# Kernel tuning notes

Hardware: AMD Instinct MI355X
Metric: run time of the kernel (lower is better)

The kernel has to match this reference:

```python
import jax, jax.numpy as jnp
import numpy as np

B, S, H, HEADS = 4, 4096, 256, 4
DH = H // HEADS
WINDOW = 16
N = B * S
EPS = 1e-5


def _build_edges():
    half = WINDOW // 2
    i = np.arange(S)
    offs = np.concatenate([np.arange(-half, 0), np.arange(1, half)])  # j in [i-half, i+half), j != i
    j = i[:, None] + offs[None, :]
    valid = (j >= 0) & (j < S)
    src_i = np.broadcast_to(i[:, None], j.shape)[valid]
    tgt_j = j[valid]
    w = (1.0 / (1.0 + np.abs(src_i - tgt_j))).astype(np.float32)
    boff = np.arange(B)[:, None] * S
    src = (boff + src_i[None, :]).reshape(-1).astype(np.int32)
    tgt = (boff + tgt_j[None, :]).reshape(-1).astype(np.int32)
    w = np.tile(w, B)
    return src, tgt, w


def setup_inputs() -> dict:
    key = jax.random.key(0)
    ks = jax.random.split(key, 8)
    src, tgt, w = _build_edges()
    sc = 0.02
    return {
        "hidden_states": jax.random.normal(ks[0], (B, S, H), jnp.float32),
        "Wc": jax.random.normal(ks[1], (H, H), jnp.float32) * sc,
        "bc": jnp.zeros((H,), jnp.float32),
        "Wa": jax.random.normal(ks[2], (H, H), jnp.float32) * sc,
        "a_src": jax.random.normal(ks[3], (HEADS, DH), jnp.float32) * sc,
        "a_tgt": jax.random.normal(ks[4], (HEADS, DH), jnp.float32) * sc,
        "ba": jnp.zeros((H,), jnp.float32),
        "ln_g": jnp.ones((H,), jnp.float32),
        "ln_b": jnp.zeros((H,), jnp.float32),
        "Wg": jax.random.normal(ks[5], (2 * H, H), jnp.float32) * sc,
        "bg": jnp.zeros((H,), jnp.float32),
        "Wp": jax.random.normal(ks[6], (H, H), jnp.float32) * sc,
        "bp": jnp.zeros((H,), jnp.float32),
        "edge_weights": jnp.asarray(w),
        "src": jnp.asarray(src),
        "tgt": jnp.asarray(tgt),
    }


def _ln(x, g, b):
    mu = jnp.mean(x, -1, keepdims=True)
    var = jnp.mean((x - mu) ** 2, -1, keepdims=True)
    return (x - mu) * jax.lax.rsqrt(var + EPS) * g + b


def reference(hidden_states, Wc, bc, Wa, a_src, a_tgt, ba, ln_g, ln_b,
              Wg, bg, Wp, bp, edge_weights, src, tgt):
    x = hidden_states.reshape(N, H)

    # --- layer 0: GraphConvolution ---
    support = x @ Wc                                   # [N,H]
    msg = edge_weights[:, None] * support[src]         # [E,H]
    gs = jax.ops.segment_sum(msg, tgt, num_segments=N) + bc
    gs = _ln(gs + x, ln_g, ln_b)

    # --- layer 1: GraphAttention (GAT-style, edge-weighted softmax) ---
    h = (gs @ Wa).reshape(N, HEADS, DH)
    es = jnp.einsum('nhd,hd->nh', h, a_src)            # [N,heads]
    et = jnp.einsum('nhd,hd->nh', h, a_tgt)
    logits = jax.nn.leaky_relu(es[src] + et[tgt], 0.2)  # [E,heads]
    m = jax.ops.segment_max(logits, tgt, num_segments=N)
    un = jnp.exp(logits - m[tgt]) * edge_weights[:, None]
    den = jax.ops.segment_sum(un, tgt, num_segments=N)
    alpha = un / (den[tgt] + 1e-9)                      # [E,heads]
    agg = jax.ops.segment_sum(alpha[:, :, None] * h[src], tgt, num_segments=N)
    gs = agg.reshape(N, H) + ba
    gs = _ln(gs + x, ln_g, ln_b)

    # --- gated integration ---
    gate = jax.nn.sigmoid(jnp.concatenate([x, gs], -1) @ Wg + bg)
    enhanced = x + gate * (gs @ Wp + bp)
    return enhanced.reshape(B, S, H)
```

## Files before the change

kernel.cpp:

```cpp
#include <hip/hip_runtime.h>
#include <math.h>

#define HD 256
#define SEQ 4096
#define NR 16384
#define NHEADS 4
#define EPSV 1e-5f
#define LDP 72
#define ZLDP 264
#define SROWS 32
#define SHALO 15
#define SLDP 264

typedef __attribute__((ext_vector_type(8))) short bf16x8;
typedef __attribute__((ext_vector_type(4))) float f32x4;

__device__ inline short f2bf(float f) {
    unsigned u = __float_as_uint(f);
    u += 0x7FFF + ((u >> 16) & 1);
    return (short)(u >> 16);
}
__device__ inline float bf2f(short s) {
    return __uint_as_float(((unsigned)(unsigned short)s) << 16);
}

__device__ inline void stage_tile(const short* __restrict__ src, int src_stride,
                                  int row0, int k0, short* lds, int rows)
{
    int t = threadIdx.x;
    int nchunk = rows >> 5;
#pragma unroll
    for (int c = 0; c < 8; ++c) {
        if (c >= nchunk) break;
        int idx = c * 256 + t;
        int r = idx >> 3, kg = idx & 7;
        bf16x8 v = *(const bf16x8*)(src + (size_t)(row0 + r) * src_stride + k0 + kg * 8);
        *(bf16x8*)(lds + r * LDP + kg * 8) = v;
    }
}

__global__ __launch_bounds__(256) void prep_w(
    const float* __restrict__ Wc, const float* __restrict__ Wa,
    const float* __restrict__ Wg, const float* __restrict__ Wp,
    short* __restrict__ WcT, short* __restrict__ WaT,
    short* __restrict__ WgT, short* __restrict__ WpT)
{
    __shared__ float lds[64][65];
    int task = blockIdx.y;
    int bx = blockIdx.x;
    int t = threadIdx.x;
    const float* W; short* Wt; int K;
    if (task == 0)      { W = Wc; Wt = WcT; K = 256; }
    else if (task == 1) { W = Wa; Wt = WaT; K = 256; }
    else if (task == 2) { W = Wg; Wt = WgT; K = 512; }
    else                { W = Wp; Wt = WpT; K = 256; }
    int ntiles = (K >> 6) * 4;
    if (bx >= ntiles) return;
    int k0 = (bx >> 2) * 64, n0 = (bx & 3) * 64;
    int ty = t >> 6, tx = t & 63;
#pragma unroll
    for (int s = 0; s < 16; ++s) {
        int r = s * 4 + ty;
        lds[r][tx] = W[(size_t)(k0 + r) * 256 + n0 + tx];
    }
    __syncthreads();
#pragma unroll
    for (int s = 0; s < 16; ++s) {
        int rn = s * 4 + ty;
        Wt[(size_t)(n0 + rn) * K + k0 + tx] = f2bf(lds[tx][rn]);
    }
}

__global__ __launch_bounds__(256) void stencil_gemm(
    const float* __restrict__ x, const short* __restrict__ WcT,
    const float* __restrict__ bc, const short* __restrict__ WaT,
    const float* __restrict__ lng, const float* __restrict__ lnb,
    const float* __restrict__ a_src, const float* __restrict__ a_tgt,
    short* __restrict__ xb, short* __restrict__ hb,
    float* __restrict__ es, float* __restrict__ et)
{
    __shared__ __align__(16) char smem[71168];
    short* lH = (short*)smem;
    short* lB = (short*)smem;
    short* lY = (short*)(smem + 36864);
    short* lZ = (short*)(smem + 53760);
    float* red_s = (float*)(smem + 70656);
    float* red_q = red_s + 64;

    int t = threadIdx.x;
    int bid = blockIdx.x;
    int swz = (bid & 7) * 64 + (bid >> 3);
    int m0 = swz * SROWS;
    int batch_base = m0 & ~(SEQ - 1);

    for (int i = t; i < (SROWS + SHALO) * 64; i += 256) {
        int r = i >> 6, c4 = (i & 63) * 4;
        int grow = m0 - 7 + r;
        short4 o4 = {0, 0, 0, 0};
        if (grow >= batch_base && grow < batch_base + SEQ) {
            float4 v = *(const float4*)(x + (size_t)grow * HD + c4);
            o4.x = f2bf(v.x); o4.y = f2bf(v.y); o4.z = f2bf(v.z); o4.w = f2bf(v.w);
        }
        *(short4*)(lH + r * SLDP + c4) = o4;
    }
    __syncthreads();
    for (int i = t; i < SROWS * 64; i += 256) {
        int r = i >> 6, c4 = (i & 63) * 4;
        *(short4*)(xb + (size_t)(m0 + r) * HD + c4) =
            *(const short4*)(lH + (r + 7) * SLDP + c4);
    }
    {
        int wv = t >> 6, ln_ = t & 63;
        int c0 = ln_ * 4;
        for (int rr = wv; rr < SROWS; rr += 4) {
            float a0 = 0.f, a1 = 0.f, a2 = 0.f, a3 = 0.f;
#pragma unroll
            for (int i = 0; i < 15; ++i) {
                int d = (i < 7) ? (i - 7) : (i - 6);
                float wd = 1.f / (1.f + (float)((d < 0) ? -d : d));
                short4 s4 = *(const short4*)(lH + (rr + 7 + d) * SLDP + c0);
                a0 += wd * bf2f(s4.x); a1 += wd * bf2f(s4.y);
                a2 += wd * bf2f(s4.z); a3 += wd * bf2f(s4.w);
            }
            short4 o;
            o.x = f2bf(a0); o.y = f2bf(a1); o.z = f2bf(a2); o.w = f2bf(a3);
            *(short4*)(lY + rr * ZLDP + c0) = o;
        }
    }

    int lane = t & 63, wid = t >> 6;
    int wm = wid & 1, wn = wid >> 1;
    int lm = lane & 15, lk = (lane >> 4) * 8;
    int rbase = (lane >> 4) * 4;

    f32x4 acc[8] = {};
    for (int kt = 0; kt < 4; ++kt) {
        __syncthreads();
        stage_tile(WcT, HD, 0, kt * 64, lB, 256);
        __syncthreads();
#pragma unroll
        for (int kk2 = 0; kk2 < 64; kk2 += 32) {
            bf16x8 a = *(const bf16x8*)(lY + (wm * 16 + lm) * ZLDP + kt * 64 + kk2 + lk);
#pragma unroll
            for (int j = 0; j < 8; ++j) {
                bf16x8 b = *(const bf16x8*)(lB + (wn * 128 + j * 16 + lm) * LDP + kk2 + lk);
                acc[j] = __builtin_amdgcn_mfma_f32_16x16x32_bf16(a, b, acc[j], 0, 0, 0);
            }
        }
    }
    float zv[8][4];
    float s4r[4] = {}, q4r[4] = {};
#pragma unroll
    for (int j = 0; j < 8; ++j)
#pragma unroll
        for (int r = 0; r < 4; ++r) {
            int n = wn * 128 + j * 16 + lm;
            int row = m0 + wm * 16 + rbase + r;
            float z = acc[j][r] + bc[n] + bf2f(xb[(size_t)row * HD + n]);
            zv[j][r] = z; s4r[r] += z; q4r[r] += z * z;
        }
#pragma unroll
    for (int r = 0; r < 4; ++r)
#pragma unroll
        for (int o = 1; o < 16; o <<= 1) {
            s4r[r] += __shfl_xor(s4r[r], o, 64);
            q4r[r] += __shfl_xor(q4r[r], o, 64);
        }
    if (lm == 0)
#pragma unroll
        for (int r = 0; r < 4; ++r) {
            red_s[wn * 32 + wm * 16 + rbase + r] = s4r[r];
            red_q[wn * 32 + wm * 16 + rbase + r] = q4r[r];
        }
    __syncthreads();
    float mu[4], inv[4];
#pragma unroll
    for (int r = 0; r < 4; ++r) {
        int rowl = wm * 16 + rbase + r;
        float S = red_s[rowl] + red_s[32 + rowl];
        float Q = red_q[rowl] + red_q[32 + rowl];
        mu[r] = S * (1.f / HD);
        inv[r] = rsqrtf(Q * (1.f / HD) - mu[r] * mu[r] + EPSV);
    }
#pragma unroll
    for (int j = 0; j < 8; ++j)
#pragma unroll
        for (int r = 0; r < 4; ++r) {
            int n = wn * 128 + j * 16 + lm;
            int rowl = wm * 16 + rbase + r;
            lZ[rowl * ZLDP + n] = f2bf((zv[j][r] - mu[r]) * inv[r] * lng[n] + lnb[n]);
        }

    f32x4 acc2[8] = {};
    for (int kt = 0; kt < 4; ++kt) {
        __syncthreads();
        stage_tile(WaT, HD, 0, kt * 64, lB, 256);
        __syncthreads();
#pragma unroll
        for (int kk2 = 0; kk2 < 64; kk2 += 32) {
            bf16x8 a = *(const bf16x8*)(lZ + (wm * 16 + lm) * ZLDP + kt * 64 + kk2 + lk);
#pragma unroll
            for (int j = 0; j < 8; ++j) {
                bf16x8 b = *(const bf16x8*)(lB + (wn * 128 + j * 16 + lm) * LDP + kk2 + lk);
                acc2[j] = __builtin_amdgcn_mfma_f32_16x16x32_bf16(a, b, acc2[j], 0, 0, 0);
            }
        }
    }
    float esA[4] = {}, etA[4] = {}, esB[4] = {}, etB[4] = {};
#pragma unroll
    for (int j = 0; j < 8; ++j) {
        int n = wn * 128 + j * 16 + lm;
        float as = a_src[n], at = a_tgt[n];
#pragma unroll
        for (int r = 0; r < 4; ++r) {
            int row = m0 + wm * 16 + rbase + r;
            hb[(size_t)row * HD + n] = f2bf(acc2[j][r]);
            if (j < 4) { esA[r] += acc2[j][r] * as; etA[r] += acc2[j][r] * at; }
            else       { esB[r] += acc2[j][r] * as; etB[r] += acc2[j][r] * at; }
        }
    }
#pragma unroll
    for (int r = 0; r < 4; ++r) {
#pragma unroll
        for (int o = 1; o < 16; o <<= 1) {
            esA[r] += __shfl_xor(esA[r], o, 64);
            etA[r] += __shfl_xor(etA[r], o, 64);
            esB[r] += __shfl_xor(esB[r], o, 64);
            etB[r] += __shfl_xor(etB[r], o, 64);
        }
        if (lm == 0) {
            int row = m0 + wm * 16 + rbase + r;
            es[row * NHEADS + wn * 2 + 0] = esA[r];
            et[row * NHEADS + wn * 2 + 0] = etA[r];
            es[row * NHEADS + wn * 2 + 1] = esB[r];
            et[row * NHEADS + wn * 2 + 1] = etB[r];
        }
    }
}

#define AF_LZ_OFF (256 * LDP * 2)
#define AF_LX_OFF (256 * LDP * 2 + 32 * ZLDP * 2)

__global__ __launch_bounds__(256) void attn_final(
    const short* __restrict__ hb, const float* __restrict__ es,
    const float* __restrict__ et, const short* __restrict__ xb,
    const float* __restrict__ ba, const float* __restrict__ lng,
    const float* __restrict__ lnb,
    const short* __restrict__ WgT, const float* __restrict__ bg,
    const short* __restrict__ WpT, const float* __restrict__ bp,
    float* __restrict__ out)
{
    __shared__ __align__(16) char smem[256 * LDP * 2 + 2 * 32 * ZLDP * 2];
    short* lH = (short*)smem;
    short* lB = (short*)smem;
    short* lZ = (short*)(smem + AF_LZ_OFF);
    short* lX = (short*)(smem + AF_LX_OFF);

    int t = threadIdx.x;
    int bid = blockIdx.x;
    int swz = (bid & 7) * 64 + (bid >> 3);
    int t0 = swz * SROWS;
    int batch_base = t0 & ~(SEQ - 1);

    for (int i = t; i < (SROWS + SHALO) * 64; i += 256) {
        int r = i >> 6, c4 = (i & 63) * 4;
        int grow = t0 - 7 + r;
        short4 v = {0, 0, 0, 0};
        if (grow >= batch_base && grow < batch_base + SEQ)
            v = *(const short4*)(hb + (size_t)grow * HD + c4);
        *(short4*)(lH + r * SLDP + c4) = v;
    }
    for (int i = t; i < SROWS * 64; i += 256) {
        int r = i >> 6, c4 = (i & 63) * 4;
        *(short4*)(lX + r * ZLDP + c4) = *(const short4*)(xb + (size_t)(t0 + r) * HD + c4);
    }
    __syncthreads();

    int wv = t >> 6, lane = t & 63;
    int tap = lane >> 2, hh = lane & 3;
    int hd = lane >> 4;
    int c0 = lane * 4;
    for (int rr = wv; rr < SROWS; rr += 4) {
        int trow = t0 + rr;
        int p = trow & (SEQ - 1);
        float lg = -1e30f, wd = 0.f;
        bool okk = false;
        if (tap < 15) {
            int d = (tap < 7) ? (tap - 7) : (tap - 6);
            int qp = p + d;
            okk = (qp >= 0) && (qp < SEQ);
            if (okk) {
                float l = es[(trow + d) * NHEADS + hh] + et[trow * NHEADS + hh];
                lg = (l > 0.f) ? l : 0.2f * l;
            }
            wd = 1.f / (1.f + (float)((d < 0) ? -d : d));
        }
        float m = lg;
#pragma unroll
        for (int o = 4; o < 64; o <<= 1) m = fmaxf(m, __shfl_xor(m, o, 64));
        float un = okk ? __expf(lg - m) * wd : 0.f;
        float den = un;
#pragma unroll
        for (int o = 4; o < 64; o <<= 1) den += __shfl_xor(den, o, 64);
        float alpha_l = un / (den + 1e-9f);

        float al[15];
#pragma unroll
        for (int i = 0; i < 15; ++i) al[i] = __shfl(alpha_l, i * 4 + hd, 64);

        float a0 = 0.f, a1 = 0.f, a2 = 0.f, a3 = 0.f;
#pragma unroll
        for (int i = 0; i < 15; ++i) {
            int d = (i < 7) ? (i - 7) : (i - 6);
            short4 s4 = *(const short4*)(lH + (rr + 7 + d) * SLDP + c0);
            a0 += al[i] * bf2f(s4.x); a1 += al[i] * bf2f(s4.y);
            a2 += al[i] * bf2f(s4.z); a3 += al[i] * bf2f(s4.w);
        }
        short4 xv4 = *(const short4*)(lX + rr * ZLDP + c0);
        float4 bav = *(const float4*)(ba + c0);
        float v0 = a0 + bav.x + bf2f(xv4.x), v1 = a1 + bav.y + bf2f(xv4.y);
        float v2 = a2 + bav.z + bf2f(xv4.z), v3 = a3 + bav.w + bf2f(xv4.w);
        float s = v0 + v1 + v2 + v3;
        float q = v0 * v0 + v1 * v1 + v2 * v2 + v3 * v3;
#pragma unroll
        for (int o = 1; o < 64; o <<= 1) { s += __shfl_xor(s, o, 64); q += __shfl_xor(q, o, 64); }
        float mu = s * (1.f / HD);
        float var = q * (1.f / HD) - mu * mu;
        float inv = rsqrtf(var + EPSV);
        float4 gv = *(const float4*)(lng + c0);
        float4 bv = *(const float4*)(lnb + c0);
        short4 o4;
        o4.x = f2bf((v0 - mu) * inv * gv.x + bv.x);
        o4.y = f2bf((v1 - mu) * inv * gv.y + bv.y);
        o4.z = f2bf((v2 - mu) * inv * gv.z + bv.z);
        o4.w = f2bf((v3 - mu) * inv * gv.w + bv.w);
        *(short4*)(lZ + rr * ZLDP + c0) = o4;
    }

    int wid = t >> 6;
    int wm = wid & 1, wn = wid >> 1;
    int lm = lane & 15, lk = (lane >> 4) * 8;
    int rbase = (lane >> 4) * 4;
    f32x4 accg[8] = {}, accp[8] = {};
    for (int kt = 0; kt < 4; ++kt) {
        __syncthreads();
        stage_tile(WgT, 512, 0, kt * 64, lB, 256);
        __syncthreads();
#pragma unroll
        for (int kk2 = 0; kk2 < 64; kk2 += 32) {
            bf16x8 a = *(const bf16x8*)(lX + (wm * 16 + lm) * ZLDP + kt * 64 + kk2 + lk);
#pragma unroll
            for (int j = 0; j < 8; ++j) {
                bf16x8 b = *(const bf16x8*)(lB + (wn * 128 + j * 16 + lm) * LDP + kk2 + lk);
                accg[j] = __builtin_amdgcn_mfma_f32_16x16x32_bf16(a, b, accg[j], 0, 0, 0);
            }
        }
    }
    for (int kt = 0; kt < 4; ++kt) {
        __syncthreads();
        stage_tile(WgT, 512, 0, 256 + kt * 64, lB, 256);
        __syncthreads();
#pragma unroll
        for (int kk2 = 0; kk2 < 64; kk2 += 32) {
            bf16x8 a = *(const bf16x8*)(lZ + (wm * 16 + lm) * ZLDP + kt * 64 + kk2 + lk);
#pragma unroll
            for (int j = 0; j < 8; ++j) {
                bf16x8 b = *(const bf16x8*)(lB + (wn * 128 + j * 16 + lm) * LDP + kk2 + lk);
                accg[j] = __builtin_amdgcn_mfma_f32_16x16x32_bf16(a, b, accg[j], 0, 0, 0);
            }
        }
    }
    for (int kt = 0; kt < 4; ++kt) {
        __syncthreads();
        stage_tile(WpT, HD, 0, kt * 64, lB, 256);
        __syncthreads();
#pragma unroll
        for (int kk2 = 0; kk2 < 64; kk2 += 32) {
            bf16x8 a = *(const bf16x8*)(lZ + (wm * 16 + lm) * ZLDP + kt * 64 + kk2 + lk);
#pragma unroll
            for (int j = 0; j < 8; ++j) {
                bf16x8 b = *(const bf16x8*)(lB + (wn * 128 + j * 16 + lm) * LDP + kk2 + lk);
                accp[j] = __builtin_amdgcn_mfma_f32_16x16x32_bf16(a, b, accp[j], 0, 0, 0);
            }
        }
    }
#pragma unroll
    for (int j = 0; j < 8; ++j)
#pragma unroll
        for (int r = 0; r < 4; ++r) {
            int n = wn * 128 + j * 16 + lm;
            int rowl = wm * 16 + rbase + r;
            size_t m = (size_t)(t0 + rowl);
            float gate = 1.f / (1.f + __expf(-(accg[j][r] + bg[n])));
            float pv = accp[j][r] + bp[n];
            out[m * HD + n] = bf2f(lX[rowl * ZLDP + n]) + gate * pv;
        }
}

extern "C" void kernel_launch(void* const* d_in, const int* in_sizes, int n_in,
                              void* d_out, int out_size, void* d_ws, size_t ws_size,
                              hipStream_t stream)
{
    const float* x     = (const float*)d_in[0];
    const float* Wc    = (const float*)d_in[1];
    const float* bc    = (const float*)d_in[2];
    const float* Wa    = (const float*)d_in[3];
    const float* a_src = (const float*)d_in[4];
    const float* a_tgt = (const float*)d_in[5];
    const float* ba    = (const float*)d_in[6];
    const float* ln_g  = (const float*)d_in[7];
    const float* ln_b  = (const float*)d_in[8];
    const float* Wg    = (const float*)d_in[9];
    const float* bg    = (const float*)d_in[10];
    const float* Wp    = (const float*)d_in[11];
    const float* bp    = (const float*)d_in[12];

    float* out = (float*)d_out;

    char* w = (char*)d_ws;
    short* xb  = (short*)w;   w += (size_t)NR * HD * 2;
    short* hb  = (short*)w;   w += (size_t)NR * HD * 2;
    float* es  = (float*)w;   w += (size_t)NR * NHEADS * 4;
    float* et  = (float*)w;   w += (size_t)NR * NHEADS * 4;
    short* WcT = (short*)w;   w += 256 * 256 * 2;
    short* WaT = (short*)w;   w += 256 * 256 * 2;
    short* WpT = (short*)w;   w += 256 * 256 * 2;
    short* WgT = (short*)w;   w += 512 * 256 * 2;

    prep_w<<<dim3(32, 4), 256, 0, stream>>>(Wc, Wa, Wg, Wp, WcT, WaT, WgT, WpT);
    stencil_gemm<<<NR / SROWS, 256, 0, stream>>>(x, WcT, bc, WaT, ln_g, ln_b,
                                                 a_src, a_tgt, xb, hb, es, et);
    attn_final<<<NR / SROWS, 256, 0, stream>>>(hb, es, et, xb, ba, ln_g, ln_b,
                                               WgT, bg, WpT, bp, out);
}
```

Measured before the change: 67.69 us.

## Double rows per block and move x-half of gate GEMM into first kernel

Rows per block go from 32 to 64, so each wave computes two 16-row MFMA tiles per staged weight tile and the weight LDS traffic per row is halved. The x·Wg[0:256] part of the gate GEMM moves into stencil_gemm, where x is already in LDS, and its result is written to a new bf16 buffer G1 that attn_final reads back in its epilogue. This rebalances work between the two kernels and removes the lX staging. The cost is an extra 8 MB round trip through global memory, higher register pressure, and half as many blocks (256), which may underfill the GPU.

```diff
diff --git a/kernel.cpp b/kernel.cpp
--- a/kernel.cpp
+++ b/kernel.cpp
@@ -8,7 +8,7 @@
 #define EPSV 1e-5f
 #define LDP 72
 #define ZLDP 264
-#define SROWS 32
+#define SROWS 64
 #define SHALO 15
 #define SLDP 264
 
@@ -24,17 +24,15 @@
     return __uint_as_float(((unsigned)(unsigned short)s) << 16);
 }
 
-__device__ inline void stage_tile(const short* __restrict__ src, int src_stride,
-                                  int row0, int k0, short* lds, int rows)
+__device__ inline void stage_w(const short* __restrict__ src, int src_stride,
+                               int k0, short* lds)
 {
     int t = threadIdx.x;
-    int nchunk = rows >> 5;
 #pragma unroll
     for (int c = 0; c < 8; ++c) {
-        if (c >= nchunk) break;
         int idx = c * 256 + t;
         int r = idx >> 3, kg = idx & 7;
-        bf16x8 v = *(const bf16x8*)(src + (size_t)(row0 + r) * src_stride + k0 + kg * 8);
+        bf16x8 v = *(const bf16x8*)(src + (size_t)r * src_stride + k0 + kg * 8);
         *(bf16x8*)(lds + r * LDP + kg * 8) = v;
     }
 }
@@ -74,22 +72,23 @@
 __global__ __launch_bounds__(256) void stencil_gemm(
     const float* __restrict__ x, const short* __restrict__ WcT,
     const float* __restrict__ bc, const short* __restrict__ WaT,
+    const short* __restrict__ WgT,
     const float* __restrict__ lng, const float* __restrict__ lnb,
     const float* __restrict__ a_src, const float* __restrict__ a_tgt,
-    short* __restrict__ xb, short* __restrict__ hb,
+    short* __restrict__ xb, short* __restrict__ hb, short* __restrict__ G1,
     float* __restrict__ es, float* __restrict__ et)
 {
-    __shared__ __align__(16) char smem[71168];
-    short* lH = (short*)smem;
-    short* lB = (short*)smem;
-    short* lY = (short*)(smem + 36864);
-    short* lZ = (short*)(smem + 53760);
-    float* red_s = (float*)(smem + 70656);
-    float* red_q = red_s + 64;
+    __shared__ __align__(16) char smem[79616];
+    short* lH  = (short*)smem;
+    short* lB1 = (short*)smem;
+    short* lB2 = (short*)(smem + 41728);
+    short* lYZ = (short*)(smem + 41728);
+    float* red_s = (float*)(smem + 78592);
+    float* red_q = red_s + 128;
 
     int t = threadIdx.x;
     int bid = blockIdx.x;
-    int swz = (bid & 7) * 64 + (bid >> 3);
+    int swz = (bid & 7) * 32 + (bid >> 3);
     int m0 = swz * SROWS;
     int batch_base = m0 & ~(SEQ - 1);
 
@@ -109,9 +108,46 @@
         *(short4*)(xb + (size_t)(m0 + r) * HD + c4) =
             *(const short4*)(lH + (r + 7) * SLDP + c4);
     }
+
+    int lane = t & 63, wid = t >> 6;
+    int wm = wid & 1, wn = wid >> 1;
+    int lm = lane & 15, lk = (lane >> 4) * 8;
+    int rbase = (lane >> 4) * 4;
+
     {
-        int wv = t >> 6, ln_ = t & 63;
-        int c0 = ln_ * 4;
+        f32x4 accG[2][8] = {};
+        for (int kt = 0; kt < 4; ++kt) {
+            __syncthreads();
+            stage_w(WgT, 512, kt * 64, lB2);
+            __syncthreads();
+#pragma unroll
+            for (int kk2 = 0; kk2 < 64; kk2 += 32) {
+                bf16x8 a[2];
+#pragma unroll
+                for (int i = 0; i < 2; ++i)
+                    a[i] = *(const bf16x8*)(lH + (7 + wm * 32 + i * 16 + lm) * SLDP + kt * 64 + kk2 + lk);
+#pragma unroll
+                for (int j = 0; j < 8; ++j) {
+                    bf16x8 b = *(const bf16x8*)(lB2 + (wn * 128 + j * 16 + lm) * LDP + kk2 + lk);
+#pragma unroll
+                    for (int i = 0; i < 2; ++i)
+                        accG[i][j] = __builtin_amdgcn_mfma_f32_16x16x32_bf16(a[i], b, accG[i][j], 0, 0, 0);
+                }
+            }
+        }
+#pragma unroll
+        for (int i = 0; i < 2; ++i)
+#pragma unroll
+            for (int j = 0; j < 8; ++j)
+#pragma unroll
+                for (int r = 0; r < 4; ++r)
+                    G1[(size_t)(m0 + wm * 32 + i * 16 + rbase + r) * HD + wn * 128 + j * 16 + lm]
+                        = f2bf(accG[i][j][r]);
+    }
+    __syncthreads();
+
+    {
+        int wv = wid, c0 = lane * 4;
         for (int rr = wv; rr < SROWS; rr += 4) {
             float a0 = 0.f, a1 = 0.f, a2 = 0.f, a3 = 0.f;
 #pragma unroll
@@ -124,141 +160,157 @@
             }
             short4 o;
             o.x = f2bf(a0); o.y = f2bf(a1); o.z = f2bf(a2); o.w = f2bf(a3);
-            *(short4*)(lY + rr * ZLDP + c0) = o;
-        }
-    }
-
-    int lane = t & 63, wid = t >> 6;
-    int wm = wid & 1, wn = wid >> 1;
-    int lm = lane & 15, lk = (lane >> 4) * 8;
-    int rbase = (lane >> 4) * 4;
-
-    f32x4 acc[8] = {};
+            *(short4*)(lYZ + rr * ZLDP + c0) = o;
+        }
+    }
+
+    f32x4 acc[2][8] = {};
     for (int kt = 0; kt < 4; ++kt) {
         __syncthreads();
-        stage_tile(WcT, HD, 0, kt * 64, lB, 256);
+        stage_w(WcT, HD, kt * 64, lB1);
         __syncthreads();
 #pragma unroll
         for (int kk2 = 0; kk2 < 64; kk2 += 32) {
-            bf16x8 a = *(const bf16x8*)(lY + (wm * 16 + lm) * ZLDP + kt * 64 + kk2 + lk);
+            bf16x8 a[2];
+#pragma unroll
+            for (int i = 0; i < 2; ++i)
+                a[i] = *(const bf16x8*)(lYZ + (wm * 32 + i * 16 + lm) * ZLDP + kt * 64 + kk2 + lk);
 #pragma unroll
             for (int j = 0; j < 8; ++j) {
-                bf16x8 b = *(const bf16x8*)(lB + (wn * 128 + j * 16 + lm) * LDP + kk2 + lk);
-                acc[j] = __builtin_amdgcn_mfma_f32_16x16x32_bf16(a, b, acc[j], 0, 0, 0);
-            }
-        }
-    }
-    float zv[8][4];
-    float s4r[4] = {}, q4r[4] = {};
-#pragma unroll
-    for (int j = 0; j < 8; ++j)
+                bf16x8 b = *(const bf16x8*)(lB1 + (wn * 128 + j * 16 + lm) * LDP + kk2 + lk);
+#pragma unroll
+                for (int i = 0; i < 2; ++i)
+                    acc[i][j] = __builtin_amdgcn_mfma_f32_16x16x32_bf16(a[i], b, acc[i][j], 0, 0, 0);
+            }
+        }
+    }
+    float zv[2][8][4];
+    float s8[2][4] = {}, q8[2][4] = {};
+#pragma unroll
+    for (int i = 0; i < 2; ++i)
+#pragma unroll
+        for (int j = 0; j < 8; ++j)
+#pragma unroll
+            for (int r = 0; r < 4; ++r) {
+                int n = wn * 128 + j * 16 + lm;
+                int row = m0 + wm * 32 + i * 16 + rbase + r;
+                float z = acc[i][j][r] + bc[n] + bf2f(xb[(size_t)row * HD + n]);
+                zv[i][j][r] = z; s8[i][r] += z; q8[i][r] += z * z;
+            }
+#pragma unroll
+    for (int i = 0; i < 2; ++i)
+#pragma unroll
+        for (int r = 0; r < 4; ++r)
+#pragma unroll
+            for (int o = 1; o < 16; o <<= 1) {
+                s8[i][r] += __shfl_xor(s8[i][r], o, 64);
+                q8[i][r] += __shfl_xor(q8[i][r], o, 64);
+            }
+    if (lm == 0)
+#pragma unroll
+        for (int i = 0; i < 2; ++i)
+#pragma unroll
+            for (int r = 0; r < 4; ++r) {
+                int rowl = wm * 32 + i * 16 + rbase + r;
+                red_s[wn * 64 + rowl] = s8[i][r];
+                red_q[wn * 64 + rowl] = q8[i][r];
+            }
+    __syncthreads();
+    float mu[2][4], inv[2][4];
+#pragma unroll
+    for (int i = 0; i < 2; ++i)
 #pragma unroll
         for (int r = 0; r < 4; ++r) {
-            int n = wn * 128 + j * 16 + lm;
-            int row = m0 + wm * 16 + rbase + r;
-            float z = acc[j][r] + bc[n] + bf2f(xb[(size_t)row * HD + n]);
-            zv[j][r] = z; s4r[r] += z; q4r[r] += z * z;
-        }
-#pragma unroll
-    for (int r = 0; r < 4; ++r)
-#pragma unroll
-        for (int o = 1; o < 16; o <<= 1) {
-            s4r[r] += __shfl_xor(s4r[r], o, 64);
-            q4r[r] += __shfl_xor(q4r[r], o, 64);
-        }
-    if (lm == 0)
-#pragma unroll
-        for (int r = 0; r < 4; ++r) {
-            red_s[wn * 32 + wm * 16 + rbase + r] = s4r[r];
-            red_q[wn * 32 + wm * 16 + rbase + r] = q4r[r];
-        }
-    __syncthreads();
-    float mu[4], inv[4];
-#pragma unroll
-    for (int r = 0; r < 4; ++r) {
-        int rowl = wm * 16 + rbase + r;
-        float S = red_s[rowl] + red_s[32 + rowl];
-        float Q = red_q[rowl] + red_q[32 + rowl];
-        mu[r] = S * (1.f / HD);
-        inv[r] = rsqrtf(Q * (1.f / HD) - mu[r] * mu[r] + EPSV);
-    }
-#pragma unroll
-    for (int j = 0; j < 8; ++j)
-#pragma unroll
-        for (int r = 0; r < 4; ++r) {
-            int n = wn * 128 + j * 16 + lm;
-            int rowl = wm * 16 + rbase + r;
-            lZ[rowl * ZLDP + n] = f2bf((zv[j][r] - mu[r]) * inv[r] * lng[n] + lnb[n]);
-        }
-
-    f32x4 acc2[8] = {};
+            int rowl = wm * 32 + i * 16 + rbase + r;
+            float S = red_s[rowl] + red_s[64 + rowl];
+            float Q = red_q[rowl] + red_q[64 + rowl];
+            mu[i][r] = S * (1.f / HD);
+            inv[i][r] = rsqrtf(Q * (1.f / HD) - mu[i][r] * mu[i][r] + EPSV);
+        }
+#pragma unroll
+    for (int i = 0; i < 2; ++i)
+#pragma unroll
+        for (int j = 0; j < 8; ++j)
+#pragma unroll
+            for (int r = 0; r < 4; ++r) {
+                int n = wn * 128 + j * 16 + lm;
+                int rowl = wm * 32 + i * 16 + rbase + r;
+                lYZ[rowl * ZLDP + n] = f2bf((zv[i][j][r] - mu[i][r]) * inv[i][r] * lng[n] + lnb[n]);
+            }
+
+    f32x4 acc2[2][8] = {};
     for (int kt = 0; kt < 4; ++kt) {
         __syncthreads();
-        stage_tile(WaT, HD, 0, kt * 64, lB, 256);
+        stage_w(WaT, HD, kt * 64, lB1);
         __syncthreads();
 #pragma unroll
         for (int kk2 = 0; kk2 < 64; kk2 += 32) {
-            bf16x8 a = *(const bf16x8*)(lZ + (wm * 16 + lm) * ZLDP + kt * 64 + kk2 + lk);
+            bf16x8 a[2];
+#pragma unroll
+            for (int i = 0; i < 2; ++i)
+                a[i] = *(const bf16x8*)(lYZ + (wm * 32 + i * 16 + lm) * ZLDP + kt * 64 + kk2 + lk);
 #pragma unroll
             for (int j = 0; j < 8; ++j) {
-                bf16x8 b = *(const bf16x8*)(lB + (wn * 128 + j * 16 + lm) * LDP + kk2 + lk);
-                acc2[j] = __builtin_amdgcn_mfma_f32_16x16x32_bf16(a, b, acc2[j], 0, 0, 0);
-            }
-        }
-    }
-    float esA[4] = {}, etA[4] = {}, esB[4] = {}, etB[4] = {};
+                bf16x8 b = *(const bf16x8*)(lB1 + (wn * 128 + j * 16 + lm) * LDP + kk2 + lk);
+#pragma unroll
+                for (int i = 0; i < 2; ++i)
+                    acc2[i][j] = __builtin_amdgcn_mfma_f32_16x16x32_bf16(a[i], b, acc2[i][j], 0, 0, 0);
+            }
+        }
+    }
+    float esA[2][4] = {}, etA[2][4] = {}, esB[2][4] = {}, etB[2][4] = {};
 #pragma unroll
     for (int j = 0; j < 8; ++j) {
         int n = wn * 128 + j * 16 + lm;
         float as = a_src[n], at = a_tgt[n];
 #pragma unroll
+        for (int i = 0; i < 2; ++i)
+#pragma unroll
+            for (int r = 0; r < 4; ++r) {
+                int row = m0 + wm * 32 + i * 16 + rbase + r;
+                hb[(size_t)row * HD + n] = f2bf(acc2[i][j][r]);
+                if (j < 4) { esA[i][r] += acc2[i][j][r] * as; etA[i][r] += acc2[i][j][r] * at; }
+                else       { esB[i][r] += acc2[i][j][r] * as; etB[i][r] += acc2[i][j][r] * at; }
+            }
+    }
+#pragma unroll
+    for (int i = 0; i < 2; ++i)
+#pragma unroll
         for (int r = 0; r < 4; ++r) {
-            int row = m0 + wm * 16 + rbase + r;
-            hb[(size_t)row * HD + n] = f2bf(acc2[j][r]);
-            if (j < 4) { esA[r] += acc2[j][r] * as; etA[r] += acc2[j][r] * at; }
-            else       { esB[r] += acc2[j][r] * as; etB[r] += acc2[j][r] * at; }
-        }
-    }
-#pragma unroll
-    for (int r = 0; r < 4; ++r) {
-#pragma unroll
-        for (int o = 1; o < 16; o <<= 1) {
-            esA[r] += __shfl_xor(esA[r], o, 64);
-            etA[r] += __shfl_xor(etA[r], o, 64);
-            esB[r] += __shfl_xor(esB[r], o, 64);
-            etB[r] += __shfl_xor(etB[r], o, 64);
-        }
-        if (lm == 0) {
-            int row = m0 + wm * 16 + rbase + r;
-            es[row * NHEADS + wn * 2 + 0] = esA[r];
-            et[row * NHEADS + wn * 2 + 0] = etA[r];
-            es[row * NHEADS + wn * 2 + 1] = esB[r];
-            et[row * NHEADS + wn * 2 + 1] = etB[r];
-        }
-    }
-}
-
-#define AF_LZ_OFF (256 * LDP * 2)
-#define AF_LX_OFF (256 * LDP * 2 + 32 * ZLDP * 2)
+#pragma unroll
+            for (int o = 1; o < 16; o <<= 1) {
+                esA[i][r] += __shfl_xor(esA[i][r], o, 64);
+                etA[i][r] += __shfl_xor(etA[i][r], o, 64);
+                esB[i][r] += __shfl_xor(esB[i][r], o, 64);
+                etB[i][r] += __shfl_xor(etB[i][r], o, 64);
+            }
+            if (lm == 0) {
+                int row = m0 + wm * 32 + i * 16 + rbase + r;
+                es[row * NHEADS + wn * 2 + 0] = esA[i][r];
+                et[row * NHEADS + wn * 2 + 0] = etA[i][r];
+                es[row * NHEADS + wn * 2 + 1] = esB[i][r];
+                et[row * NHEADS + wn * 2 + 1] = etB[i][r];
+            }
+        }
+}
 
 __global__ __launch_bounds__(256) void attn_final(
     const short* __restrict__ hb, const float* __restrict__ es,
     const float* __restrict__ et, const short* __restrict__ xb,
-    const float* __restrict__ ba, const float* __restrict__ lng,
-    const float* __restrict__ lnb,
+    const short* __restrict__ G1, const float* __restrict__ ba,
+    const float* __restrict__ lng, const float* __restrict__ lnb,
     const short* __restrict__ WgT, const float* __restrict__ bg,
     const short* __restrict__ WpT, const float* __restrict__ bp,
     float* __restrict__ out)
 {
-    __shared__ __align__(16) char smem[256 * LDP * 2 + 2 * 32 * ZLDP * 2];
+    __shared__ __align__(16) char smem[75520];
     short* lH = (short*)smem;
     short* lB = (short*)smem;
-    short* lZ = (short*)(smem + AF_LZ_OFF);
-    short* lX = (short*)(smem + AF_LX_OFF);
+    short* lZ = (short*)(smem + 41728);
 
     int t = threadIdx.x;
     int bid = blockIdx.x;
-    int swz = (bid & 7) * 64 + (bid >> 3);
+    int swz = (bid & 7) * 32 + (bid >> 3);
     int t0 = swz * SROWS;
     int batch_base = t0 & ~(SEQ - 1);
 
@@ -269,10 +321,6 @@
         if (grow >= batch_base && grow < batch_base + SEQ)
             v = *(const short4*)(hb + (size_t)grow * HD + c4);
         *(short4*)(lH + r * SLDP + c4) = v;
-    }
-    for (int i = t; i < SROWS * 64; i += 256) {
-        int r = i >> 6, c4 = (i & 63) * 4;
-        *(short4*)(lX + r * ZLDP + c4) = *(const short4*)(xb + (size_t)(t0 + r) * HD + c4);
     }
     __syncthreads();
 
@@ -316,7 +364,7 @@
             a0 += al[i] * bf2f(s4.x); a1 += al[i] * bf2f(s4.y);
             a2 += al[i] * bf2f(s4.z); a3 += al[i] * bf2f(s4.w);
         }
-        short4 xv4 = *(const short4*)(lX + rr * ZLDP + c0);
+        short4 xv4 = *(const short4*)(xb + (size_t)trow * HD + c0);
         float4 bav = *(const float4*)(ba + c0);
         float v0 = a0 + bav.x + bf2f(xv4.x), v1 = a1 + bav.y + bf2f(xv4.y);
         float v2 = a2 + bav.z + bf2f(xv4.z), v3 = a3 + bav.w + bf2f(xv4.w);
@@ -341,60 +389,58 @@
     int wm = wid & 1, wn = wid >> 1;
     int lm = lane & 15, lk = (lane >> 4) * 8;
     int rbase = (lane >> 4) * 4;
-    f32x4 accg[8] = {}, accp[8] = {};
+    f32x4 accg[2][8] = {}, accp[2][8] = {};
     for (int kt = 0; kt < 4; ++kt) {
         __syncthreads();
-        stage_tile(WgT, 512, 0, kt * 64, lB, 256);
+        stage_w(WgT, 512, 256 + kt * 64, lB);
         __syncthreads();
 #pragma unroll
         for (int kk2 = 0; kk2 < 64; kk2 += 32) {
-            bf16x8 a = *(const bf16x8*)(lX + (wm * 16 + lm) * ZLDP + kt * 64 + kk2 + lk);
+            bf16x8 a[2];
+#pragma unroll
+            for (int i = 0; i < 2; ++i)
+                a[i] = *(const bf16x8*)(lZ + (wm * 32 + i * 16 + lm) * ZLDP + kt * 64 + kk2 + lk);
 #pragma unroll
             for (int j = 0; j < 8; ++j) {
                 bf16x8 b = *(const bf16x8*)(lB + (wn * 128 + j * 16 + lm) * LDP + kk2 + lk);
-                accg[j] = __builtin_amdgcn_mfma_f32_16x16x32_bf16(a, b, accg[j], 0, 0, 0);
+#pragma unroll
+                for (int i = 0; i < 2; ++i)
+                    accg[i][j] = __builtin_amdgcn_mfma_f32_16x16x32_bf16(a[i], b, accg[i][j], 0, 0, 0);
             }
         }
     }
     for (int kt = 0; kt < 4; ++kt) {
         __syncthreads();
-        stage_tile(WgT, 512, 0, 256 + kt * 64, lB, 256);
+        stage_w(WpT, HD, kt * 64, lB);
         __syncthreads();
 #pragma unroll
         for (int kk2 = 0; kk2 < 64; kk2 += 32) {
-            bf16x8 a = *(const bf16x8*)(lZ + (wm * 16 + lm) * ZLDP + kt * 64 + kk2 + lk);
+            bf16x8 a[2];
+#pragma unroll
+            for (int i = 0; i < 2; ++i)
+                a[i] = *(const bf16x8*)(lZ + (wm * 32 + i * 16 + lm) * ZLDP + kt * 64 + kk2 + lk);
 #pragma unroll
             for (int j = 0; j < 8; ++j) {
                 bf16x8 b = *(const bf16x8*)(lB + (wn * 128 + j * 16 + lm) * LDP + kk2 + lk);
-                accg[j] = __builtin_amdgcn_mfma_f32_16x16x32_bf16(a, b, accg[j], 0, 0, 0);
-            }
-        }
-    }
-    for (int kt = 0; kt < 4; ++kt) {
-        __syncthreads();
-        stage_tile(WpT, HD, 0, kt * 64, lB, 256);
-        __syncthreads();
-#pragma unroll
-        for (int kk2 = 0; kk2 < 64; kk2 += 32) {
-            bf16x8 a = *(const bf16x8*)(lZ + (wm * 16 + lm) * ZLDP + kt * 64 + kk2 + lk);
-#pragma unroll
-            for (int j = 0; j < 8; ++j) {
-                bf16x8 b = *(const bf16x8*)(lB + (wn * 128 + j * 16 + lm) * LDP + kk2 + lk);
-                accp[j] = __builtin_amdgcn_mfma_f32_16x16x32_bf16(a, b, accp[j], 0, 0, 0);
-            }
-        }
-    }
-#pragma unroll
-    for (int j = 0; j < 8; ++j)
-#pragma unroll
-        for (int r = 0; r < 4; ++r) {
-            int n = wn * 128 + j * 16 + lm;
-            int rowl = wm * 16 + rbase + r;
-            size_t m = (size_t)(t0 + rowl);
-            float gate = 1.f / (1.f + __expf(-(accg[j][r] + bg[n])));
-            float pv = accp[j][r] + bp[n];
-            out[m * HD + n] = bf2f(lX[rowl * ZLDP + n]) + gate * pv;
-        }
+#pragma unroll
+                for (int i = 0; i < 2; ++i)
+                    accp[i][j] = __builtin_amdgcn_mfma_f32_16x16x32_bf16(a[i], b, accp[i][j], 0, 0, 0);
+            }
+        }
+    }
+#pragma unroll
+    for (int i = 0; i < 2; ++i)
+#pragma unroll
+        for (int j = 0; j < 8; ++j)
+#pragma unroll
+            for (int r = 0; r < 4; ++r) {
+                int n = wn * 128 + j * 16 + lm;
+                size_t m = (size_t)(t0 + wm * 32 + i * 16 + rbase + r);
+                float g1 = bf2f(G1[m * HD + n]);
+                float gate = 1.f / (1.f + __expf(-(accg[i][j][r] + g1 + bg[n])));
+                float pv = accp[i][j][r] + bp[n];
+                out[m * HD + n] = bf2f(xb[m * HD + n]) + gate * pv;
+            }
 }
 
 extern "C" void kernel_launch(void* const* d_in, const int* in_sizes, int n_in,
@@ -420,6 +466,7 @@
     char* w = (char*)d_ws;
     short* xb  = (short*)w;   w += (size_t)NR * HD * 2;
     short* hb  = (short*)w;   w += (size_t)NR * HD * 2;
+    short* G1  = (short*)w;   w += (size_t)NR * HD * 2;
     float* es  = (float*)w;   w += (size_t)NR * NHEADS * 4;
     float* et  = (float*)w;   w += (size_t)NR * NHEADS * 4;
     short* WcT = (short*)w;   w += 256 * 256 * 2;
@@ -428,8 +475,8 @@
     short* WgT = (short*)w;   w += 512 * 256 * 2;
 
     prep_w<<<dim3(32, 4), 256, 0, stream>>>(Wc, Wa, Wg, Wp, WcT, WaT, WgT, WpT);
-    stencil_gemm<<<NR / SROWS, 256, 0, stream>>>(x, WcT, bc, WaT, ln_g, ln_b,
-                                                 a_src, a_tgt, xb, hb, es, et);
-    attn_final<<<NR / SROWS, 256, 0, stream>>>(hb, es, et, xb, ba, ln_g, ln_b,
+    stencil_gemm<<<NR / SROWS, 256, 0, stream>>>(x, WcT, bc, WaT, WgT, ln_g, ln_b,
+                                                 a_src, a_tgt, xb, hb, G1, es, et);
+    attn_final<<<NR / SROWS, 256, 0, stream>>>(hb, es, et, xb, G1, ba, ln_g, ln_b,
                                                WgT, bg, WpT, bp, out);
 }
```

After: 112.4 us. 1.66x slower.
